# Optimization experiments

Hardware: AMD Instinct MI355X
Metric: run time of the kernel (lower is better)

## Reference

```python
import jax, jax.numpy as jnp
import numpy as np

B, T, C = 2, 2048, 1024
H = 16
HD = C // H  # 64


def setup_inputs() -> dict:
    key = jax.random.key(0)
    k1, k2, k3, k4, k5 = jax.random.split(key, 5)
    s = 0.02
    return {
        "x": jax.random.normal(k1, (B, T, C), dtype=jnp.float32),
        "w_attn": jax.random.normal(k2, (C, 3 * C), dtype=jnp.float32) * s,
        "b_attn": jnp.zeros((3 * C,), dtype=jnp.float32),
        "w_proj": jax.random.normal(k3, (C, C), dtype=jnp.float32) * s,
        "b_proj": jnp.zeros((C,), dtype=jnp.float32),
    }


def reference(x, w_attn, b_attn, w_proj, b_proj):
    Bx, Tx, Cx = x.shape
    qkv = x @ w_attn + b_attn                      # [B,T,3C]
    q, k, v = jnp.split(qkv, 3, axis=-1)
    # [B,T,C] -> [B,H,T,HD]
    def heads(t):
        return t.reshape(Bx, Tx, H, HD).transpose(0, 2, 1, 3)
    q, k, v = heads(q), heads(k), heads(v)
    scale = 1.0 / np.sqrt(HD).astype(np.float32)
    scores = jnp.einsum("bhqd,bhkd->bhqk", q, k) * scale
    causal = jnp.tril(jnp.ones((Tx, Tx), dtype=bool))
    scores = jnp.where(causal, scores, -jnp.inf)
    attn = jax.nn.softmax(scores, axis=-1)          # dropout p=0 -> identity
    y = jnp.einsum("bhqk,bhkd->bhqd", attn, v)
    y = y.transpose(0, 2, 1, 3).reshape(Bx, Tx, Cx)
    return y @ w_proj + b_proj
```

## Files before the change

kernel.cpp:

```cpp
#include <hip/hip_runtime.h>
#include <hip/hip_bf16.h>

#define Bb 2
#define Tt 2048
#define Cc 1024
#define Hh 16
#define HD 64
#define QS 0.18033688f

typedef __attribute__((ext_vector_type(8))) short bf16x8;
typedef __attribute__((ext_vector_type(4))) short bf16x4;
typedef __attribute__((ext_vector_type(4))) float f32x4;
typedef __attribute__((ext_vector_type(2))) unsigned int u32x2;

__device__ inline short f2b(float f) {
    unsigned int u = __builtin_bit_cast(unsigned int, f);
    unsigned int r = (u + 0x7FFFu + ((u >> 16) & 1u)) >> 16;
    return (short)(unsigned short)r;
}

__device__ inline void gl16(const void* g, void* l) {
    __builtin_amdgcn_global_load_lds(
        (const __attribute__((address_space(1))) void*)g,
        (__attribute__((address_space(3))) void*)l, 16, 0, 0);
}

__global__ __launch_bounds__(256) void prep_kernel(
    const float* __restrict__ x, short* __restrict__ xbf,
    const float* __restrict__ wA, short* __restrict__ wAT,
    const float* __restrict__ wP, short* __restrict__ wPT)
{
    const int bx = blockIdx.x, tid = threadIdx.x;
    if (bx < 2048) {
        int i = (bx * 256 + tid) * 8;
        float4 a = *(const float4*)(x + i);
        float4 b = *(const float4*)(x + i + 4);
        bf16x8 v;
        v[0] = f2b(a.x); v[1] = f2b(a.y); v[2] = f2b(a.z); v[3] = f2b(a.w);
        v[4] = f2b(b.x); v[5] = f2b(b.y); v[6] = f2b(b.z); v[7] = f2b(b.w);
        *(bf16x8*)(xbf + i) = v;
        return;
    }
    const float* W; short* WT; int N, t;
    if (bx < 2816) { t = bx - 2048; W = wA; WT = wAT; N = 3072; }
    else           { t = bx - 2816; W = wP; WT = wPT; N = 1024; }
    const int K = 1024;
    int k0 = (t & 15) * 64, n0 = (t >> 4) * 64;
    int nl = tid & 63, kg = tid >> 6;
    int n = n0 + nl;
    short v[16];
#pragma unroll
    for (int i = 0; i < 16; i++)
        v[i] = f2b(W[(size_t)(k0 + kg * 16 + i) * N + n]);
    short* dst = WT + (size_t)n * K + k0 + kg * 16;
    *(bf16x8*)dst = *(bf16x8*)&v[0];
    *(bf16x8*)(dst + 8) = *(bf16x8*)&v[8];
}

__global__ __launch_bounds__(256) void gemm_qkv(
    const short* __restrict__ A, const short* __restrict__ Bt,
    const float* __restrict__ bias,
    short* __restrict__ qw, short* __restrict__ kw, short* __restrict__ vTw,
    int M, int N, int K)
{
    __shared__ __attribute__((aligned(16))) short SH[17408];

    const int tid  = threadIdx.x;
    const int wave = tid >> 6, lane = tid & 63;
    const int quad = lane >> 4, lr = lane & 15;
    const int wm = wave >> 1, wn = wave & 1;
    const int m0 = blockIdx.y * 128, n0 = blockIdx.x * 128;

    int srow[2], scol[2];
#pragma unroll
    for (int i = 0; i < 2; i++) {
        int id = i * 256 + tid;
        srow[i] = id >> 2;
        scol[i] = ((id & 3) ^ ((srow[i] >> 1) & 3)) << 3;
    }
    const int pfrag = quad ^ ((lr >> 1) & 3);

    f32x4 acc[4][4];
    const f32x4 zf = {0.f, 0.f, 0.f, 0.f};
#pragma unroll
    for (int mi = 0; mi < 4; mi++)
#pragma unroll
        for (int ni = 0; ni < 4; ni++) acc[mi][ni] = zf;

#pragma unroll
    for (int i = 0; i < 2; i++) {
        gl16(A + (size_t)(m0 + srow[i]) * K + scol[i], &SH[(i * 256 + tid) * 8]);
        gl16(Bt + (size_t)(n0 + srow[i]) * K + scol[i], &SH[8192 + (i * 256 + tid) * 8]);
    }

    const int iters = K >> 5;
    for (int it = 0; it < iters; ++it) {
        const int co = (it & 1) * 4096;
        const int no = ((it & 1) ^ 1) * 4096;
        __syncthreads();
        if (it + 1 < iters) {
            const int k1 = (it + 1) << 5;
#pragma unroll
            for (int i = 0; i < 2; i++) {
                gl16(A + (size_t)(m0 + srow[i]) * K + k1 + scol[i],
                     &SH[no + (i * 256 + tid) * 8]);
                gl16(Bt + (size_t)(n0 + srow[i]) * K + k1 + scol[i],
                     &SH[8192 + no + (i * 256 + tid) * 8]);
            }
        }
        bf16x8 af[4], bf[4];
#pragma unroll
        for (int mi = 0; mi < 4; mi++) {
            int row = wm * 64 + mi * 16 + lr;
            af[mi] = *(bf16x8*)&SH[co + (row * 4 + pfrag) * 8];
        }
#pragma unroll
        for (int ni = 0; ni < 4; ni++) {
            int row = wn * 64 + ni * 16 + lr;
            bf[ni] = *(bf16x8*)&SH[8192 + co + (row * 4 + pfrag) * 8];
        }
#pragma unroll
        for (int mi = 0; mi < 4; mi++)
#pragma unroll
            for (int ni = 0; ni < 4; ni++)
                acc[mi][ni] = __builtin_amdgcn_mfma_f32_16x16x32_bf16(
                    af[mi], bf[ni], acc[mi][ni], 0, 0, 0);
    }

    if (n0 < 2048) {
#pragma unroll
        for (int mi = 0; mi < 4; mi++) {
#pragma unroll
            for (int ni = 0; ni < 4; ni++) {
                int c = n0 + wn * 64 + ni * 16 + lr;
                float bv = bias[c];
#pragma unroll
                for (int r = 0; r < 4; r++) {
                    int rg = m0 + wm * 64 + mi * 16 + quad * 4 + r;
                    float val = acc[mi][ni][r] + bv;
                    int which = c >> 10, cc = c & 1023;
                    int h = cc >> 6, d = cc & 63;
                    int b = rg >> 11, t = rg & 2047;
                    size_t bh = (size_t)b * Hh + h;
                    if (which == 0) qw[(bh * Tt + t) * HD + d] = f2b(val * QS);
                    else            kw[(bh * Tt + t) * HD + d] = f2b(val);
                }
            }
        }
    } else {
        __syncthreads();
#pragma unroll
        for (int ni = 0; ni < 4; ni++) {
            int cl = wn * 64 + ni * 16 + lr;
            float bv = bias[n0 + cl];
#pragma unroll
            for (int mi = 0; mi < 4; mi++)
#pragma unroll
                for (int r = 0; r < 4; r++) {
                    int tl = wm * 64 + mi * 16 + quad * 4 + r;
                    SH[cl * 136 + tl] = f2b(acc[mi][ni][r] + bv);
                }
        }
        __syncthreads();
        const int rl = tid >> 1, half = tid & 1;
        const int cc = (n0 & 1023) + rl;
        const int h = cc >> 6, d = cc & 63;
        const int b = m0 >> 11, tb = (m0 & 2047) + half * 64;
        short* dst = vTw + (((size_t)b * Hh + h) * HD + d) * Tt + tb;
        const short* src = &SH[rl * 136 + half * 64];
#pragma unroll
        for (int jj = 0; jj < 8; jj++)
            *(bf16x8*)(dst + jj * 8) = *(const bf16x8*)(src + jj * 8);
    }
}

__global__ __launch_bounds__(256) void gemm_proj(
    const short* __restrict__ A, const short* __restrict__ Bt,
    const float* __restrict__ bias, float* __restrict__ out,
    int M, int N, int K)
{
    __shared__ __attribute__((aligned(16))) short SH[12288];

    const int tid  = threadIdx.x;
    const int wave = tid >> 6, lane = tid & 63;
    const int quad = lane >> 4, lr = lane & 15;
    const int wm = wave >> 1, wn = wave & 1;
    const int m0 = blockIdx.y * 64, n0 = blockIdx.x * 128;

    const int arow = tid >> 2;
    const int acol = ((tid & 3) ^ ((arow >> 1) & 3)) << 3;
    int brow[2], bcol[2];
#pragma unroll
    for (int i = 0; i < 2; i++) {
        int id = i * 256 + tid;
        brow[i] = id >> 2;
        bcol[i] = ((id & 3) ^ ((brow[i] >> 1) & 3)) << 3;
    }
    const int pfrag = quad ^ ((lr >> 1) & 3);

    f32x4 acc[2][4];
    const f32x4 zf = {0.f, 0.f, 0.f, 0.f};
#pragma unroll
    for (int mi = 0; mi < 2; mi++)
#pragma unroll
        for (int ni = 0; ni < 4; ni++) acc[mi][ni] = zf;

    auto asrc = [&](int row, int col) -> const short* {
        int rg = m0 + row, b = rg >> 11, t = rg & 2047;
        int h = col >> 6, d = col & 63;
        return A + ((((size_t)b * Hh + h) * Tt + t) * HD + d);
    };

    gl16(asrc(arow, acol), &SH[tid * 8]);
#pragma unroll
    for (int i = 0; i < 2; i++)
        gl16(Bt + (size_t)(n0 + brow[i]) * K + bcol[i],
             &SH[4096 + (i * 256 + tid) * 8]);

    const int iters = K >> 5;
    for (int it = 0; it < iters; ++it) {
        const int coA = (it & 1) * 2048, noA = ((it & 1) ^ 1) * 2048;
        const int coB = (it & 1) * 4096, noB = ((it & 1) ^ 1) * 4096;
        __syncthreads();
        if (it + 1 < iters) {
            const int k1 = (it + 1) << 5;
            gl16(asrc(arow, k1 + acol), &SH[noA + tid * 8]);
#pragma unroll
            for (int i = 0; i < 2; i++)
                gl16(Bt + (size_t)(n0 + brow[i]) * K + k1 + bcol[i],
                     &SH[4096 + noB + (i * 256 + tid) * 8]);
        }
        bf16x8 af[2], bf[4];
#pragma unroll
        for (int mi = 0; mi < 2; mi++) {
            int row = wm * 32 + mi * 16 + lr;
            af[mi] = *(bf16x8*)&SH[coA + (row * 4 + pfrag) * 8];
        }
#pragma unroll
        for (int ni = 0; ni < 4; ni++) {
            int row = wn * 64 + ni * 16 + lr;
            bf[ni] = *(bf16x8*)&SH[4096 + coB + (row * 4 + pfrag) * 8];
        }
#pragma unroll
        for (int mi = 0; mi < 2; mi++)
#pragma unroll
            for (int ni = 0; ni < 4; ni++)
                acc[mi][ni] = __builtin_amdgcn_mfma_f32_16x16x32_bf16(
                    af[mi], bf[ni], acc[mi][ni], 0, 0, 0);
    }

#pragma unroll
    for (int mi = 0; mi < 2; mi++)
#pragma unroll
        for (int ni = 0; ni < 4; ni++) {
            int c = n0 + wn * 64 + ni * 16 + lr;
            float bv = bias[c];
#pragma unroll
            for (int r = 0; r < 4; r++) {
                int rg = m0 + wm * 32 + mi * 16 + quad * 4 + r;
                out[(size_t)rg * N + c] = acc[mi][ni][r] + bv;
            }
        }
}

__global__ __launch_bounds__(256) void gemm_f32src(
    const void* __restrict__ Araw, const float* __restrict__ Bm,
    const float* __restrict__ bias, float* __restrict__ out,
    short* __restrict__ qw, short* __restrict__ kw, short* __restrict__ vTw,
    int M, int N, int K, int mode)
{
    __shared__ __attribute__((aligned(16))) short As[128 * 32];
    __shared__ __attribute__((aligned(16))) short Bs[128 * 32];

    const int tid  = threadIdx.x;
    const int wave = tid >> 6, lane = tid & 63;
    const int quad = lane >> 4, lr = lane & 15;
    const int wm = wave >> 1, wn = wave & 1;
    const int m0 = blockIdx.y * 128, n0 = blockIdx.x * 128;

    f32x4 acc[4][4];
    const f32x4 zf = {0.f, 0.f, 0.f, 0.f};
#pragma unroll
    for (int mi = 0; mi < 4; mi++)
#pragma unroll
        for (int ni = 0; ni < 4; ni++) acc[mi][ni] = zf;

    for (int k0 = 0; k0 < K; k0 += 32) {
        __syncthreads();
        if (mode == 1) {
            const float* Af = (const float*)Araw;
#pragma unroll
            for (int i = 0; i < 4; i++) {
                int id  = i * 256 + tid;
                int row = id >> 3;
                int kc  = (id & 7) << 2;
                float4 v = *(const float4*)(Af + (size_t)(m0 + row) * K + k0 + kc);
                short* d = &As[row * 32 + kc];
                d[0] = f2b(v.x); d[1] = f2b(v.y); d[2] = f2b(v.z); d[3] = f2b(v.w);
            }
        } else {
            const short* Ah = (const short*)Araw;
#pragma unroll
            for (int i = 0; i < 2; i++) {
                int id  = i * 256 + tid;
                int row = id >> 2;
                int kc  = (id & 3) << 3;
                int rg = m0 + row, b = rg >> 11, t = rg & 2047;
                int c = k0 + kc, h = c >> 6, d = c & 63;
                *(bf16x8*)&As[row * 32 + kc] =
                    *(const bf16x8*)(Ah + ((((size_t)b * Hh + h) * Tt + t) * HD + d));
            }
        }
#pragma unroll
        for (int i = 0; i < 4; i++) {
            int id = i * 256 + tid;
            int kr = id >> 5;
            int nc = (id & 31) << 2;
            float4 v = *(const float4*)(Bm + (size_t)(k0 + kr) * N + n0 + nc);
            Bs[(nc + 0) * 32 + kr] = f2b(v.x);
            Bs[(nc + 1) * 32 + kr] = f2b(v.y);
            Bs[(nc + 2) * 32 + kr] = f2b(v.z);
            Bs[(nc + 3) * 32 + kr] = f2b(v.w);
        }
        __syncthreads();

        bf16x8 af[4], bf[4];
#pragma unroll
        for (int mi = 0; mi < 4; mi++)
            af[mi] = *(bf16x8*)&As[(wm * 64 + mi * 16 + lr) * 32 + quad * 8];
#pragma unroll
        for (int ni = 0; ni < 4; ni++)
            bf[ni] = *(bf16x8*)&Bs[(wn * 64 + ni * 16 + lr) * 32 + quad * 8];
#pragma unroll
        for (int mi = 0; mi < 4; mi++)
#pragma unroll
            for (int ni = 0; ni < 4; ni++)
                acc[mi][ni] = __builtin_amdgcn_mfma_f32_16x16x32_bf16(
                    af[mi], bf[ni], acc[mi][ni], 0, 0, 0);
    }

#pragma unroll
    for (int mi = 0; mi < 4; mi++) {
#pragma unroll
        for (int ni = 0; ni < 4; ni++) {
            int c = n0 + wn * 64 + ni * 16 + lr;
            float bv = bias[c];
#pragma unroll
            for (int r = 0; r < 4; r++) {
                int rg = m0 + wm * 64 + mi * 16 + quad * 4 + r;
                float val = acc[mi][ni][r] + bv;
                if (mode == 1) {
                    int which = c >> 10, cc = c & 1023;
                    int h = cc >> 6, d = cc & 63;
                    int b = rg >> 11, t = rg & 2047;
                    size_t bh = (size_t)b * Hh + h;
                    if (which == 0)      qw[(bh * Tt + t) * HD + d] = f2b(val * QS);
                    else if (which == 1) kw[(bh * Tt + t) * HD + d] = f2b(val);
                    else                 vTw[(bh * HD + d) * Tt + t] = f2b(val);
                } else {
                    out[(size_t)rg * N + c] = val;
                }
            }
        }
    }
}

__global__ __launch_bounds__(256) void attn_kernel(
    short* __restrict__ qw, const short* __restrict__ kw,
    const short* __restrict__ vTw)
{
    __shared__ __attribute__((aligned(16))) short Ks[2][8192];
    __shared__ __attribute__((aligned(16))) short Vs[2][8192];

    const int bh = blockIdx.x & 31;
    const int g  = blockIdx.x >> 5;
    const int tid = threadIdx.x;
    const int wave = tid >> 6, lane = tid & 63;
    const int quad = lane >> 4, lr = lane & 15;

    const int pA = 2 * g + (wave >> 1);
    const int pB = 63 - pA;
    const int wh = (wave & 1) * 16;
    const int r0m[2] = { pA * 32 + wh, pB * 32 + wh };

    short* qp = qw + (size_t)bh * Tt * HD;
    const short* kp = kw + (size_t)bh * Tt * HD;
    const short* vp = vTw + (size_t)bh * HD * Tt;

    int krow[4], kcol[4], vrow[4], vcol[4];
#pragma unroll
    for (int i = 0; i < 4; i++) {
        int id = i * 256 + tid;
        krow[i] = id >> 3;
        kcol[i] = ((id & 7) ^ (krow[i] & 7)) << 3;
        vrow[i] = id >> 4;
        vcol[i] = ((id & 15) ^ (vrow[i] & 15)) << 3;
    }

    const int kb0b = lr * 64 + ((quad     ^ (lr & 7)) << 3);
    const int kb1b = lr * 64 + (((4 + quad) ^ (lr & 7)) << 3);
    const int qh = quad >> 1, ql = quad & 1;
    int vbase[4];
#pragma unroll
    for (int nt = 0; nt < 4; nt++)
        vbase[nt] = (nt * 16 + lr) * 128 + ql * 4;

    bf16x8 aq[2][2];
#pragma unroll
    for (int mt = 0; mt < 2; mt++)
#pragma unroll
        for (int h = 0; h < 2; h++)
            aq[mt][h] = *(const bf16x8*)(qp + (size_t)(r0m[mt] + lr) * HD
                                            + h * 32 + quad * 8);

    const f32x4 zf = {0.f, 0.f, 0.f, 0.f};
    f32x4 o[2][4];
    float lacc[2] = {0.f, 0.f};
#pragma unroll
    for (int mt = 0; mt < 2; mt++)
#pragma unroll
        for (int nt = 0; nt < 4; nt++) o[mt][nt] = zf;

#pragma unroll
    for (int i = 0; i < 4; i++) {
        gl16(kp + (size_t)krow[i] * HD + kcol[i], &Ks[0][(i * 256 + tid) * 8]);
        gl16(vp + (size_t)vrow[i] * Tt + vcol[i], &Vs[0][(i * 256 + tid) * 8]);
    }

    const int clast = ((63 - 2 * g) * 32 + 31) >> 7;
    for (int c = 0; c <= clast; ++c) {
        const int j0 = c << 7;
        const int cur = c & 1;
        __syncthreads();
        if (c < clast) {
#pragma unroll
            for (int i = 0; i < 4; i++) {
                gl16(kp + (size_t)(j0 + 128 + krow[i]) * HD + kcol[i],
                     &Ks[cur ^ 1][(i * 256 + tid) * 8]);
                gl16(vp + (size_t)vrow[i] * Tt + (j0 + 128) + vcol[i],
                     &Vs[cur ^ 1][(i * 256 + tid) * 8]);
            }
        }
        const short* Kc = &Ks[cur][0];
        const short* Vc = &Vs[cur][0];
        __builtin_amdgcn_s_setprio(1);
#pragma unroll
        for (int kt = 0; kt < 8; kt++) {
            const int k16 = j0 + kt * 16;
            const bool act0 = k16 <= r0m[0] + 15;
            const bool act1 = k16 <= r0m[1] + 15;
            if (!act1 && !act0) break;
            bf16x8 kb0 = *(const bf16x8*)&Kc[kt * 1024 + kb0b];
            bf16x8 kb1 = *(const bf16x8*)&Kc[kt * 1024 + kb1b];
            const int sl8 = (((kt * 2 + qh) ^ lr) << 3);
            bf16x4 va[4];
#pragma unroll
            for (int nt = 0; nt < 4; nt++)
                va[nt] = *(const bf16x4*)&Vc[vbase[nt] + sl8];
#pragma unroll
            for (int mt = 0; mt < 2; mt++) {
                if (!(mt ? act1 : act0)) continue;
                f32x4 s = __builtin_amdgcn_mfma_f32_16x16x32_bf16(
                    kb0, aq[mt][0], zf, 0, 0, 0);
                s = __builtin_amdgcn_mfma_f32_16x16x32_bf16(
                    kb1, aq[mt][1], s, 0, 0, 0);
                unsigned u[4];
                if (k16 + 15 <= r0m[mt]) {
#pragma unroll
                    for (int r = 0; r < 4; r++) {
                        float e = __builtin_amdgcn_exp2f(s[r]);
                        u[r] = __builtin_bit_cast(unsigned, e);
                        lacc[mt] += e;
                    }
                } else {
#pragma unroll
                    for (int r = 0; r < 4; r++) {
                        float e = __builtin_amdgcn_exp2f(s[r]);
                        if ((k16 + quad * 4 + r) > (r0m[mt] + lr)) e = 0.f;
                        u[r] = __builtin_bit_cast(unsigned, e);
                        lacc[mt] += e;
                    }
                }
                u32x2 pu = { __builtin_amdgcn_perm(u[1], u[0], 0x07060302u),
                             __builtin_amdgcn_perm(u[3], u[2], 0x07060302u) };
                bf16x4 pt = __builtin_bit_cast(bf16x4, pu);
#pragma unroll
                for (int nt = 0; nt < 4; nt++)
                    o[mt][nt] = __builtin_amdgcn_mfma_f32_16x16x16bf16_1k(
                        va[nt], pt, o[mt][nt], 0, 0, 0);
            }
        }
        __builtin_amdgcn_s_setprio(0);
    }

#pragma unroll
    for (int mt = 0; mt < 2; mt++) {
        lacc[mt] += __shfl_xor(lacc[mt], 16, 64);
        lacc[mt] += __shfl_xor(lacc[mt], 32, 64);
        lacc[mt] = 1.0f / lacc[mt];
    }

#pragma unroll
    for (int mt = 0; mt < 2; mt++)
#pragma unroll
        for (int nt = 0; nt < 4; nt++) {
            bf16x4 ov;
#pragma unroll
            for (int r = 0; r < 4; r++) ov[r] = f2b(o[mt][nt][r] * lacc[mt]);
            *(bf16x4*)(qp + (size_t)(r0m[mt] + lr) * HD + nt * 16 + quad * 4) = ov;
        }
}

extern "C" void kernel_launch(void* const* d_in, const int* in_sizes, int n_in,
                              void* d_out, int out_size, void* d_ws, size_t ws_size,
                              hipStream_t stream) {
    const float* x      = (const float*)d_in[0];
    const float* w_attn = (const float*)d_in[1];
    const float* b_attn = (const float*)d_in[2];
    const float* w_proj = (const float*)d_in[3];
    const float* b_proj = (const float*)d_in[4];
    float* out = (float*)d_out;

    const size_t per = (size_t)Bb * Hh * Tt * HD;
    short* qw  = (short*)d_ws;
    short* kw  = qw + per;
    short* vTw = kw + per;
    const int M = Bb * Tt;

    const size_t need_fast = (3 * per + per + (size_t)3072 * 1024 + (size_t)1024 * 1024) * 2;

    if (ws_size >= need_fast) {
        short* xbf = vTw + per;
        short* wAT = xbf + per;
        short* wPT = wAT + (size_t)3072 * 1024;

        prep_kernel<<<dim3(3072), 256, 0, stream>>>(x, xbf, w_attn, wAT, w_proj, wPT);

        gemm_qkv<<<dim3(3 * Cc / 128, M / 128), 256, 0, stream>>>(
            xbf, wAT, b_attn, qw, kw, vTw, M, 3 * Cc, Cc);

        attn_kernel<<<dim3(512), 256, 0, stream>>>(qw, kw, vTw);

        gemm_proj<<<dim3(Cc / 128, M / 64), 256, 0, stream>>>(
            qw, wPT, b_proj, out, M, Cc, Cc);
    } else {
        gemm_f32src<<<dim3(3 * Cc / 128, M / 128), 256, 0, stream>>>(
            x, w_attn, b_attn, nullptr, qw, kw, vTw, M, 3 * Cc, Cc, 1);

        attn_kernel<<<dim3(512), 256, 0, stream>>>(qw, kw, vTw);

        gemm_f32src<<<dim3(Cc / 128, M / 128), 256, 0, stream>>>(
            qw, w_proj, b_proj, out, nullptr, nullptr, nullptr, M, Cc, Cc, 2);
    }
}
```

Before: 184.2 us.

## Rewrite QKV GEMM with 256x256 tiles and a four-phase software pipeline

The QKV projection GEMM moves from 128x128 tiles with 256 threads to 256x256 tiles with 512 threads (8 waves) and a K-step of 64. Global-to-LDS loads are double-buffered and split into four quarter-tile phases, with explicit vmcnt waits, raw s_barrier and setprio around the MFMA bursts, plus a swizzled block-to-tile mapping. The goal is to raise MFMA density, reuse each staged tile more, and overlap loads with compute. The grid shrinks to 192 blocks, each using 128 KB of LDS, which may leave CUs idle and cap occupancy at one block per CU. The V-transpose epilogue now runs in two passes to fit the wider tile.

```diff
diff --git a/kernel.cpp b/kernel.cpp
--- a/kernel.cpp
+++ b/kernel.cpp
@@ -57,120 +57,153 @@
     *(bf16x8*)(dst + 8) = *(bf16x8*)&v[8];
 }
 
-__global__ __launch_bounds__(256) void gemm_qkv(
+#define VM4 asm volatile("s_waitcnt vmcnt(4)" ::: "memory")
+#define VM2 asm volatile("s_waitcnt vmcnt(2)" ::: "memory")
+#define VM0 asm volatile("s_waitcnt vmcnt(0)" ::: "memory")
+#define VMN (void)0
+#define BARRIER asm volatile("s_barrier" ::: "memory")
+
+#define STG_A(nb, h, kb) { \
+    gl16(A + baA[h] + (kb), &LB[(((nb) << 1) | (h)) * 8192 + dst8]); \
+    gl16(A + baA[h] + 131072 + (kb), &LB[(((nb) << 1) | (h)) * 8192 + dst8 + 4096]); }
+#define STG_B(nb, h, kb) { \
+    gl16(Bt + baB[h] + (kb), &LB[32768 + (((nb) << 1) | (h)) * 8192 + dst8]); \
+    gl16(Bt + baB[h] + 131072 + (kb), &LB[32768 + (((nb) << 1) | (h)) * 8192 + dst8 + 4096]); }
+
+#define PHASE(bb, MH, NH, STG, WAIT) { \
+    WAIT; \
+    BARRIER; \
+    const short* Ab_ = &LB[(((bb) << 1) | (MH)) * 8192]; \
+    const short* Bb_ = &LB[32768 + (((bb) << 1) | (NH)) * 8192]; \
+    bf16x8 af_[4][2], bf_[2][2]; \
+    _Pragma("unroll") for (int f_ = 0; f_ < 4; f_++) \
+        _Pragma("unroll") for (int kh_ = 0; kh_ < 2; kh_++) \
+            af_[f_][kh_] = *(const bf16x8*)&Ab_[aro[f_] + kx[kh_]]; \
+    _Pragma("unroll") for (int e_ = 0; e_ < 2; e_++) \
+        _Pragma("unroll") for (int kh_ = 0; kh_ < 2; kh_++) \
+            bf_[e_][kh_] = *(const bf16x8*)&Bb_[bro[e_] + kx[kh_]]; \
+    STG; \
+    __builtin_amdgcn_s_setprio(1); \
+    _Pragma("unroll") for (int f_ = 0; f_ < 4; f_++) \
+        _Pragma("unroll") for (int e_ = 0; e_ < 2; e_++) \
+            _Pragma("unroll") for (int kh_ = 0; kh_ < 2; kh_++) \
+                acc[(MH) * 4 + f_][(NH) * 2 + e_] = \
+                    __builtin_amdgcn_mfma_f32_16x16x32_bf16( \
+                        af_[f_][kh_], bf_[e_][kh_], \
+                        acc[(MH) * 4 + f_][(NH) * 2 + e_], 0, 0, 0); \
+    __builtin_amdgcn_s_setprio(0); }
+
+__global__ __launch_bounds__(512, 2) void gemm_qkv(
     const short* __restrict__ A, const short* __restrict__ Bt,
     const float* __restrict__ bias,
     short* __restrict__ qw, short* __restrict__ kw, short* __restrict__ vTw,
     int M, int N, int K)
 {
-    __shared__ __attribute__((aligned(16))) short SH[17408];
+    __shared__ __attribute__((aligned(16))) short LB[65536];
 
     const int tid  = threadIdx.x;
     const int wave = tid >> 6, lane = tid & 63;
     const int quad = lane >> 4, lr = lane & 15;
-    const int wm = wave >> 1, wn = wave & 1;
-    const int m0 = blockIdx.y * 128, n0 = blockIdx.x * 128;
-
-    int srow[2], scol[2];
-#pragma unroll
-    for (int i = 0; i < 2; i++) {
-        int id = i * 256 + tid;
-        srow[i] = id >> 2;
-        scol[i] = ((id & 3) ^ ((srow[i] >> 1) & 3)) << 3;
-    }
-    const int pfrag = quad ^ ((lr >> 1) & 3);
-
-    f32x4 acc[4][4];
+    const int wm = wave >> 2, wn = wave & 3;
+
+    const int bid = blockIdx.x;
+    const int sw = (bid & 7) * 24 + (bid >> 3);
+    const int bx = sw % 12, by = sw / 12;
+    const int m0 = by * 256, n0 = bx * 256;
+
+    const int dst8 = tid * 8;
+    size_t baA[2], baB[2];
+    {
+        int r = tid >> 3;
+        int cs = ((tid & 7) ^ (r & 7)) << 3;
+#pragma unroll
+        for (int h = 0; h < 2; h++) {
+            int gA = m0 + ((r >> 6) << 7) + h * 64 + (r & 63);
+            int gB = n0 + ((r >> 5) << 6) + h * 32 + (r & 31);
+            baA[h] = (size_t)gA * 1024 + cs;
+            baB[h] = (size_t)gB * 1024 + cs;
+        }
+    }
+
+    int aro[4], bro[2], kx[2];
+#pragma unroll
+    for (int f = 0; f < 4; f++) aro[f] = (wm * 64 + f * 16 + lr) * 64;
+#pragma unroll
+    for (int e = 0; e < 2; e++) bro[e] = (wn * 32 + e * 16 + lr) * 64;
+#pragma unroll
+    for (int kh = 0; kh < 2; kh++)
+        kx[kh] = (((kh * 4 + quad) ^ (lr & 7)) << 3);
+
+    f32x4 acc[8][4];
     const f32x4 zf = {0.f, 0.f, 0.f, 0.f};
 #pragma unroll
-    for (int mi = 0; mi < 4; mi++)
-#pragma unroll
-        for (int ni = 0; ni < 4; ni++) acc[mi][ni] = zf;
-
-#pragma unroll
-    for (int i = 0; i < 2; i++) {
-        gl16(A + (size_t)(m0 + srow[i]) * K + scol[i], &SH[(i * 256 + tid) * 8]);
-        gl16(Bt + (size_t)(n0 + srow[i]) * K + scol[i], &SH[8192 + (i * 256 + tid) * 8]);
-    }
-
-    const int iters = K >> 5;
-    for (int it = 0; it < iters; ++it) {
-        const int co = (it & 1) * 4096;
-        const int no = ((it & 1) ^ 1) * 4096;
-        __syncthreads();
-        if (it + 1 < iters) {
-            const int k1 = (it + 1) << 5;
-#pragma unroll
-            for (int i = 0; i < 2; i++) {
-                gl16(A + (size_t)(m0 + srow[i]) * K + k1 + scol[i],
-                     &SH[no + (i * 256 + tid) * 8]);
-                gl16(Bt + (size_t)(n0 + srow[i]) * K + k1 + scol[i],
-                     &SH[8192 + no + (i * 256 + tid) * 8]);
-            }
-        }
-        bf16x8 af[4], bf[4];
-#pragma unroll
-        for (int mi = 0; mi < 4; mi++) {
-            int row = wm * 64 + mi * 16 + lr;
-            af[mi] = *(bf16x8*)&SH[co + (row * 4 + pfrag) * 8];
-        }
-#pragma unroll
-        for (int ni = 0; ni < 4; ni++) {
-            int row = wn * 64 + ni * 16 + lr;
-            bf[ni] = *(bf16x8*)&SH[8192 + co + (row * 4 + pfrag) * 8];
-        }
-#pragma unroll
-        for (int mi = 0; mi < 4; mi++)
-#pragma unroll
-            for (int ni = 0; ni < 4; ni++)
-                acc[mi][ni] = __builtin_amdgcn_mfma_f32_16x16x32_bf16(
-                    af[mi], bf[ni], acc[mi][ni], 0, 0, 0);
-    }
+    for (int mf = 0; mf < 8; mf++)
+#pragma unroll
+        for (int nf = 0; nf < 4; nf++) acc[mf][nf] = zf;
+
+    STG_A(0, 0, 0); STG_B(0, 0, 0); STG_A(0, 1, 0); STG_B(0, 1, 0);
+
+    for (int t = 0; t < 15; ++t) {
+        const int bb = t & 1, nb = bb ^ 1;
+        const int kb1 = (t + 1) << 6;
+        PHASE(bb, 0, 0, STG_A(nb, 0, kb1), VM4);
+        PHASE(bb, 1, 0, STG_B(nb, 0, kb1), VM4);
+        PHASE(bb, 0, 1, STG_A(nb, 1, kb1), VM4);
+        PHASE(bb, 1, 1, STG_B(nb, 1, kb1), VMN);
+    }
+    PHASE(1, 0, 0, VMN, VM4);
+    PHASE(1, 1, 0, VMN, VM2);
+    PHASE(1, 0, 1, VMN, VM0);
+    PHASE(1, 1, 1, VMN, VMN);
 
     if (n0 < 2048) {
 #pragma unroll
-        for (int mi = 0; mi < 4; mi++) {
-#pragma unroll
-            for (int ni = 0; ni < 4; ni++) {
-                int c = n0 + wn * 64 + ni * 16 + lr;
-                float bv = bias[c];
+        for (int nf = 0; nf < 4; nf++) {
+            int c = n0 + wn * 64 + nf * 16 + lr;
+            float bv = bias[c];
+            int which = c >> 10, cc = c & 1023;
+            int h = cc >> 6, d = cc & 63;
+            short* base = which ? kw : qw;
+            float qs = which ? 1.0f : QS;
+#pragma unroll
+            for (int mf = 0; mf < 8; mf++)
 #pragma unroll
                 for (int r = 0; r < 4; r++) {
-                    int rg = m0 + wm * 64 + mi * 16 + quad * 4 + r;
-                    float val = acc[mi][ni][r] + bv;
-                    int which = c >> 10, cc = c & 1023;
-                    int h = cc >> 6, d = cc & 63;
-                    int b = rg >> 11, t = rg & 2047;
-                    size_t bh = (size_t)b * Hh + h;
-                    if (which == 0) qw[(bh * Tt + t) * HD + d] = f2b(val * QS);
-                    else            kw[(bh * Tt + t) * HD + d] = f2b(val);
+                    int rg = m0 + wm * 128 + mf * 16 + quad * 4 + r;
+                    int b = rg >> 11, tq = rg & 2047;
+                    float val = acc[mf][nf][r] + bv;
+                    base[(((size_t)b * Hh + h) * Tt + tq) * HD + d] = f2b(val * qs);
                 }
-            }
         }
     } else {
-        __syncthreads();
-#pragma unroll
-        for (int ni = 0; ni < 4; ni++) {
-            int cl = wn * 64 + ni * 16 + lr;
-            float bv = bias[n0 + cl];
-#pragma unroll
-            for (int mi = 0; mi < 4; mi++)
-#pragma unroll
-                for (int r = 0; r < 4; r++) {
-                    int tl = wm * 64 + mi * 16 + quad * 4 + r;
-                    SH[cl * 136 + tl] = f2b(acc[mi][ni][r] + bv);
+#pragma unroll
+        for (int p = 0; p < 2; p++) {
+            __syncthreads();
+            if ((wn >> 1) == p) {
+#pragma unroll
+                for (int nf = 0; nf < 4; nf++) {
+                    int cl = (wn & 1) * 64 + nf * 16 + lr;
+                    float bv = bias[n0 + p * 128 + cl];
+#pragma unroll
+                    for (int mf = 0; mf < 8; mf++)
+#pragma unroll
+                        for (int r = 0; r < 4; r++) {
+                            int tl = wm * 128 + mf * 16 + quad * 4 + r;
+                            LB[cl * 264 + tl] = f2b(acc[mf][nf][r] + bv);
+                        }
                 }
-        }
-        __syncthreads();
-        const int rl = tid >> 1, half = tid & 1;
-        const int cc = (n0 & 1023) + rl;
-        const int h = cc >> 6, d = cc & 63;
-        const int b = m0 >> 11, tb = (m0 & 2047) + half * 64;
-        short* dst = vTw + (((size_t)b * Hh + h) * HD + d) * Tt + tb;
-        const short* src = &SH[rl * 136 + half * 64];
-#pragma unroll
-        for (int jj = 0; jj < 8; jj++)
-            *(bf16x8*)(dst + jj * 8) = *(const bf16x8*)(src + jj * 8);
+            }
+            __syncthreads();
+            const int rl = tid >> 2, seg = tid & 3;
+            const int cc = (n0 & 1023) + p * 128 + rl;
+            const int h = cc >> 6, d = cc & 63;
+            const int b2 = m0 >> 11, tb = (m0 & 2047) + seg * 64;
+            short* dstv = vTw + (((size_t)b2 * Hh + h) * HD + d) * Tt + tb;
+            const short* srcv = &LB[rl * 264 + seg * 64];
+#pragma unroll
+            for (int jj = 0; jj < 8; jj++)
+                *(bf16x8*)(dstv + jj * 8) = *(const bf16x8*)(srcv + jj * 8);
+        }
     }
 }
 
@@ -536,7 +569,7 @@
 
         prep_kernel<<<dim3(3072), 256, 0, stream>>>(x, xbf, w_attn, wAT, w_proj, wPT);
 
-        gemm_qkv<<<dim3(3 * Cc / 128, M / 128), 256, 0, stream>>>(
+        gemm_qkv<<<dim3(192), 512, 0, stream>>>(
             xbf, wAT, b_attn, qw, kw, vTw, M, 3 * Cc, Cc);
 
         attn_kernel<<<dim3(512), 256, 0, stream>>>(qw, kw, vTw);
```

Result: no change. 186.0 us (+0.9%).

## Restructure QKV GEMM with K=64 tiles, interleaved LDS reads and block swizzle

Applied to the files above, without the earlier changes.

Rewrites the QKV projection GEMM main loop to stage 64-wide K tiles into a double-buffered 64KB LDS region with an XOR swizzle. It interleaves LDS fragment reads with MFMA quadrants under raised wave priority, and uses explicit waitcnt/barrier plus a sched_barrier. The grid is flattened to 1D and remapped so consecutive blocks group by XCD (bid&7) for cache locality, with launch_bounds(256,2). This halves barrier count and aims to overlap global loads with compute, at the cost of more LDS per block, which may limit occupancy, and hardcoded K=1024 assumptions.

```diff
diff --git a/kernel.cpp b/kernel.cpp
--- a/kernel.cpp
+++ b/kernel.cpp
@@ -57,87 +57,125 @@
     *(bf16x8*)(dst + 8) = *(bf16x8*)&v[8];
 }
 
-__global__ __launch_bounds__(256) void gemm_qkv(
+#define VM0 asm volatile("s_waitcnt vmcnt(0)" ::: "memory")
+#define BARRIER asm volatile("s_barrier" ::: "memory")
+#define SCHEDB __builtin_amdgcn_sched_barrier(0)
+
+#define STG(nb, kb) { \
+    gl16(A + baA0 + (kb), &LB[((nb) << 1) * 4096 + dst8]); \
+    gl16(A + baA0 + 32768 + (kb), &LB[((nb) << 1) * 4096 + 2048 + dst8]); \
+    gl16(A + baA1 + (kb), &LB[(((nb) << 1) | 1) * 4096 + dst8]); \
+    gl16(A + baA1 + 32768 + (kb), &LB[(((nb) << 1) | 1) * 4096 + 2048 + dst8]); \
+    gl16(Bt + baB0 + (kb), &LB[16384 + ((nb) << 1) * 4096 + dst8]); \
+    gl16(Bt + baB0 + 32768 + (kb), &LB[16384 + ((nb) << 1) * 4096 + 2048 + dst8]); \
+    gl16(Bt + baB1 + (kb), &LB[16384 + (((nb) << 1) | 1) * 4096 + dst8]); \
+    gl16(Bt + baB1 + 32768 + (kb), &LB[16384 + (((nb) << 1) | 1) * 4096 + 2048 + dst8]); }
+
+#define RD_A(bb, flo) { \
+    const short* Ab_ = &LB[(((bb) << 1) | wm) * 4096]; \
+    _Pragma("unroll") for (int f_ = 0; f_ < 2; f_++) \
+        _Pragma("unroll") for (int kh_ = 0; kh_ < 2; kh_++) \
+            af[(flo) + f_][kh_] = *(const bf16x8*)&Ab_[aro[(flo) + f_] + kx[kh_]]; }
+
+#define RD_B(bb, elo) { \
+    const short* Bb_ = &LB[16384 + (((bb) << 1) | wn) * 4096]; \
+    _Pragma("unroll") for (int e_ = 0; e_ < 2; e_++) \
+        _Pragma("unroll") for (int kh_ = 0; kh_ < 2; kh_++) \
+            bf[(elo) + e_][kh_] = *(const bf16x8*)&Bb_[bro[(elo) + e_] + kx[kh_]]; }
+
+#define QMM(FH, EH) { \
+    __builtin_amdgcn_s_setprio(1); \
+    _Pragma("unroll") for (int f_ = 0; f_ < 2; f_++) \
+        _Pragma("unroll") for (int e_ = 0; e_ < 2; e_++) \
+            _Pragma("unroll") for (int kh_ = 0; kh_ < 2; kh_++) \
+                acc[(FH) * 2 + f_][(EH) * 2 + e_] = \
+                    __builtin_amdgcn_mfma_f32_16x16x32_bf16( \
+                        af[(FH) * 2 + f_][kh_], bf[(EH) * 2 + e_][kh_], \
+                        acc[(FH) * 2 + f_][(EH) * 2 + e_], 0, 0, 0); \
+    __builtin_amdgcn_s_setprio(0); }
+
+#define TILE(bb, nb, kb1) { \
+    RD_A(bb, 0); RD_B(bb, 0); \
+    STG(nb, kb1); \
+    QMM(0, 0); \
+    RD_B(bb, 2); QMM(0, 1); \
+    RD_A(bb, 2); QMM(1, 1); \
+    QMM(1, 0); \
+    VM0; BARRIER; SCHEDB; }
+
+#define TILE_LAST(bb) { \
+    RD_A(bb, 0); RD_B(bb, 0); \
+    QMM(0, 0); \
+    RD_B(bb, 2); QMM(0, 1); \
+    RD_A(bb, 2); QMM(1, 1); \
+    QMM(1, 0); }
+
+__global__ __launch_bounds__(256, 2) void gemm_qkv(
     const short* __restrict__ A, const short* __restrict__ Bt,
     const float* __restrict__ bias,
     short* __restrict__ qw, short* __restrict__ kw, short* __restrict__ vTw,
     int M, int N, int K)
 {
-    __shared__ __attribute__((aligned(16))) short SH[17408];
+    __shared__ __attribute__((aligned(16))) short LB[32768];
 
     const int tid  = threadIdx.x;
     const int wave = tid >> 6, lane = tid & 63;
     const int quad = lane >> 4, lr = lane & 15;
     const int wm = wave >> 1, wn = wave & 1;
-    const int m0 = blockIdx.y * 128, n0 = blockIdx.x * 128;
-
-    int srow[2], scol[2];
-#pragma unroll
-    for (int i = 0; i < 2; i++) {
-        int id = i * 256 + tid;
-        srow[i] = id >> 2;
-        scol[i] = ((id & 3) ^ ((srow[i] >> 1) & 3)) << 3;
-    }
-    const int pfrag = quad ^ ((lr >> 1) & 3);
+
+    const int bid = blockIdx.x;
+    const int sw = (bid & 7) * 96 + (bid >> 3);
+    const int bx = sw % 24, by = sw / 24;
+    const int m0 = by * 128, n0 = bx * 128;
+
+    const int dst8 = tid * 8;
+    const int cs = ((tid & 7) ^ ((tid >> 3) & 7)) << 3;
+    const size_t baA0 = (size_t)(m0 + (tid >> 3)) * 1024 + cs;
+    const size_t baA1 = (size_t)(m0 + 64 + (tid >> 3)) * 1024 + cs;
+    const size_t baB0 = (size_t)(n0 + (tid >> 3)) * 1024 + cs;
+    const size_t baB1 = (size_t)(n0 + 64 + (tid >> 3)) * 1024 + cs;
+
+    int aro[4], bro[4], kx[2];
+#pragma unroll
+    for (int f = 0; f < 4; f++) {
+        aro[f] = (f * 16 + lr) * 64;
+        bro[f] = (f * 16 + lr) * 64;
+    }
+#pragma unroll
+    for (int kh = 0; kh < 2; kh++)
+        kx[kh] = (((kh * 4 + quad) ^ (lr & 7)) << 3);
 
     f32x4 acc[4][4];
     const f32x4 zf = {0.f, 0.f, 0.f, 0.f};
 #pragma unroll
-    for (int mi = 0; mi < 4; mi++)
-#pragma unroll
-        for (int ni = 0; ni < 4; ni++) acc[mi][ni] = zf;
-
-#pragma unroll
-    for (int i = 0; i < 2; i++) {
-        gl16(A + (size_t)(m0 + srow[i]) * K + scol[i], &SH[(i * 256 + tid) * 8]);
-        gl16(Bt + (size_t)(n0 + srow[i]) * K + scol[i], &SH[8192 + (i * 256 + tid) * 8]);
-    }
-
-    const int iters = K >> 5;
-    for (int it = 0; it < iters; ++it) {
-        const int co = (it & 1) * 4096;
-        const int no = ((it & 1) ^ 1) * 4096;
-        __syncthreads();
-        if (it + 1 < iters) {
-            const int k1 = (it + 1) << 5;
-#pragma unroll
-            for (int i = 0; i < 2; i++) {
-                gl16(A + (size_t)(m0 + srow[i]) * K + k1 + scol[i],
-                     &SH[no + (i * 256 + tid) * 8]);
-                gl16(Bt + (size_t)(n0 + srow[i]) * K + k1 + scol[i],
-                     &SH[8192 + no + (i * 256 + tid) * 8]);
-            }
-        }
-        bf16x8 af[4], bf[4];
-#pragma unroll
-        for (int mi = 0; mi < 4; mi++) {
-            int row = wm * 64 + mi * 16 + lr;
-            af[mi] = *(bf16x8*)&SH[co + (row * 4 + pfrag) * 8];
-        }
-#pragma unroll
-        for (int ni = 0; ni < 4; ni++) {
-            int row = wn * 64 + ni * 16 + lr;
-            bf[ni] = *(bf16x8*)&SH[8192 + co + (row * 4 + pfrag) * 8];
-        }
-#pragma unroll
-        for (int mi = 0; mi < 4; mi++)
-#pragma unroll
-            for (int ni = 0; ni < 4; ni++)
-                acc[mi][ni] = __builtin_amdgcn_mfma_f32_16x16x32_bf16(
-                    af[mi], bf[ni], acc[mi][ni], 0, 0, 0);
-    }
+    for (int mf = 0; mf < 4; mf++)
+#pragma unroll
+        for (int nf = 0; nf < 4; nf++) acc[mf][nf] = zf;
+
+    bf16x8 af[4][2], bf[4][2];
+
+    STG(0, 0);
+    VM0;
+    BARRIER;
+
+    for (int it = 0; it < 7; ++it) {
+        TILE(0, 1, (2 * it + 1) << 6);
+        TILE(1, 0, (2 * it + 2) << 6);
+    }
+    TILE(0, 1, 15 << 6);
+    TILE_LAST(1);
 
     if (n0 < 2048) {
 #pragma unroll
-        for (int mi = 0; mi < 4; mi++) {
-#pragma unroll
-            for (int ni = 0; ni < 4; ni++) {
-                int c = n0 + wn * 64 + ni * 16 + lr;
+        for (int nf = 0; nf < 4; nf++) {
+#pragma unroll
+            for (int mf = 0; mf < 4; mf++) {
+                int c = n0 + wn * 64 + nf * 16 + lr;
                 float bv = bias[c];
 #pragma unroll
                 for (int r = 0; r < 4; r++) {
-                    int rg = m0 + wm * 64 + mi * 16 + quad * 4 + r;
-                    float val = acc[mi][ni][r] + bv;
+                    int rg = m0 + wm * 64 + mf * 16 + quad * 4 + r;
+                    float val = acc[mf][nf][r] + bv;
                     int which = c >> 10, cc = c & 1023;
                     int h = cc >> 6, d = cc & 63;
                     int b = rg >> 11, t = rg & 2047;
@@ -150,15 +188,15 @@
     } else {
         __syncthreads();
 #pragma unroll
-        for (int ni = 0; ni < 4; ni++) {
-            int cl = wn * 64 + ni * 16 + lr;
+        for (int nf = 0; nf < 4; nf++) {
+            int cl = wn * 64 + nf * 16 + lr;
             float bv = bias[n0 + cl];
 #pragma unroll
-            for (int mi = 0; mi < 4; mi++)
+            for (int mf = 0; mf < 4; mf++)
 #pragma unroll
                 for (int r = 0; r < 4; r++) {
-                    int tl = wm * 64 + mi * 16 + quad * 4 + r;
-                    SH[cl * 136 + tl] = f2b(acc[mi][ni][r] + bv);
+                    int tl = wm * 64 + mf * 16 + quad * 4 + r;
+                    LB[cl * 136 + tl] = f2b(acc[mf][nf][r] + bv);
                 }
         }
         __syncthreads();
@@ -167,7 +205,7 @@
         const int h = cc >> 6, d = cc & 63;
         const int b = m0 >> 11, tb = (m0 & 2047) + half * 64;
         short* dst = vTw + (((size_t)b * Hh + h) * HD + d) * Tt + tb;
-        const short* src = &SH[rl * 136 + half * 64];
+        const short* src = &LB[rl * 136 + half * 64];
 #pragma unroll
         for (int jj = 0; jj < 8; jj++)
             *(bf16x8*)(dst + jj * 8) = *(const bf16x8*)(src + jj * 8);
@@ -536,7 +574,7 @@
 
         prep_kernel<<<dim3(3072), 256, 0, stream>>>(x, xbf, w_attn, wAT, w_proj, wPT);
 
-        gemm_qkv<<<dim3(3 * Cc / 128, M / 128), 256, 0, stream>>>(
+        gemm_qkv<<<dim3(768), 256, 0, stream>>>(
             xbf, wAT, b_attn, qw, kw, vTw, M, 3 * Cc, Cc);
 
         attn_kernel<<<dim3(512), 256, 0, stream>>>(qw, kw, vTw);
```

Result: faster. 174.9 us (-5.1%).
